# Kernel optimization log

Hardware: AMD Instinct MI355X
Metric: run time of the kernel (lower is better)

The kernel has to match this reference:

```python
import jax, jax.numpy as jnp
import numpy as np

B = 8192
NUM_NODES = 100000
EMB = 128
W1D, W2D, W3D = 64, 128, 256   # witness_dims
CODE = 128
HID = 64                        # hardcoded hidden_dim in WitnessExtractor / decoder
TOTW = W1D + W2D + W3D          # 448


def _linear_params(key, fan_in, fan_out):
    k1, k2 = jax.random.split(key)
    bound = 1.0 / np.sqrt(fan_in)
    w = jax.random.uniform(k1, (fan_out, fan_in), jnp.float32, -bound, bound)
    b = jax.random.uniform(k2, (fan_out,), jnp.float32, -bound, bound)
    return w, b


def setup_inputs() -> dict:
    key = jax.random.key(0)
    ks = jax.random.split(key, 12)
    u = jax.random.randint(ks[0], (B,), 0, NUM_NODES, dtype=jnp.int64 if jax.config.jax_enable_x64 else jnp.int32)
    v = jax.random.randint(ks[1], (B,), 0, NUM_NODES, dtype=u.dtype)
    emb = jax.random.normal(ks[2], (NUM_NODES, EMB), jnp.float32)
    e1_w1, e1_b1 = _linear_params(ks[3], 2 * EMB, HID)
    e1_w2, e1_b2 = _linear_params(ks[4], HID, W1D)
    e2_w1, e2_b1 = _linear_params(ks[5], 2 * EMB + W1D, HID)
    e2_w2, e2_b2 = _linear_params(ks[6], HID, W2D)
    e3_w1, e3_b1 = _linear_params(ks[7], 2 * EMB + W2D, HID)
    e3_w2, e3_b2 = _linear_params(ks[8], HID, W3D)
    trop_w = jax.random.normal(ks[9], (CODE, TOTW), jnp.float32)  # init_scale=1.0
    dec_w1, dec_b1 = _linear_params(ks[10], CODE, HID)
    dec_w2, dec_b2 = _linear_params(ks[11], HID, 1)
    return dict(u=u, v=v, emb=emb,
                e1_w1=e1_w1, e1_b1=e1_b1, e1_w2=e1_w2, e1_b2=e1_b2,
                e2_w1=e2_w1, e2_b1=e2_b1, e2_w2=e2_w2, e2_b2=e2_b2,
                e3_w1=e3_w1, e3_b1=e3_b1, e3_w2=e3_w2, e3_b2=e3_b2,
                trop_w=trop_w, dec_w1=dec_w1, dec_b1=dec_b1,
                dec_w2=dec_w2, dec_b2=dec_b2)


def _witness(x, w1, b1, w2, b2):
    h = jax.nn.relu(x @ w1.T + b1)
    return jax.nn.sigmoid(h @ w2.T + b2)


def reference(u, v, emb,
              e1_w1, e1_b1, e1_w2, e1_b2,
              e2_w1, e2_b1, e2_w2, e2_b2,
              e3_w1, e3_b1, e3_w2, e3_b2,
              trop_w, dec_w1, dec_b1, dec_w2, dec_b2):
    u_emb = emb[u]                               # [B, EMB]
    v_emb = emb[v]
    base = jnp.concatenate([u_emb, v_emb], axis=1)  # [B, 2*EMB]
    w1 = _witness(base, e1_w1, e1_b1, e1_w2, e1_b2)
    w2 = _witness(jnp.concatenate([base, w1], axis=1), e2_w1, e2_b1, e2_w2, e2_b2)
    w3 = _witness(jnp.concatenate([base, w2], axis=1), e3_w1, e3_b1, e3_w2, e3_b2)
    wit = jnp.concatenate([w1, w2, w3], axis=1)  # [B, TOTW]
    # tropical (min-plus) matmul: code[b,o] = min_j (wit[b,j] + trop_w[o,j])
    code = jnp.min(wit[:, None, :] + trop_w[None, :, :], axis=2)  # [B, CODE]
    h = jax.nn.relu(code @ dec_w1.T + dec_b1)
    return h @ dec_w2.T + dec_b2                 # [B, 1]
```

## Files before the change

kernel.cpp:

```cpp
#include <hip/hip_runtime.h>
#include <hip/hip_fp16.h>
#include <math.h>

#define BATCH 8192
#define EMB 128
#define TILE 16
#define NTHREADS 1024
#define NWAVES 16
#define CH 136
#define WITS 450
#define ENT_CAP 4096

#define OFF_E1W1 0
#define OFF_E1W2 16384
#define OFF_E2W1 20480
#define OFF_E2W2 40960
#define OFF_E3W1 49152
#define OFF_E3W2 73728
#define OFF_DW1  90112
#define OFF_DW2  98304
#define W_DENSE  98368

typedef __attribute__((ext_vector_type(8))) _Float16 v8h;
typedef __attribute__((ext_vector_type(4))) float v4f;

struct Smem {
    _Float16 XB[32 * CH];
    _Float16 W12C[24 * CH];
    _Float16 H[8 * CH];
    _Float16 CODE[16 * CH];
    _Float16 WITrm[TILE * WITS];
    unsigned int ent[ENT_CAP];
    unsigned int off[132];
};

__global__ __launch_bounds__(1024) void prep_kernel(
    const float* __restrict__ s0, const float* __restrict__ s1,
    const float* __restrict__ s2, const float* __restrict__ s3,
    const float* __restrict__ s4, const float* __restrict__ s5,
    const float* __restrict__ s6, const float* __restrict__ s7,
    const float* __restrict__ trop, _Float16* __restrict__ ws)
{
    const int b = blockIdx.x;
    const int tid = threadIdx.x;
    if (b < 25) {
        const int idx4 = (b * 1024 + tid) * 4;
        if (idx4 >= W_DENSE) return;
        const float* src; int off;
        if      (idx4 < OFF_E1W2) { src = s0; off = OFF_E1W1; }
        else if (idx4 < OFF_E2W1) { src = s1; off = OFF_E1W2; }
        else if (idx4 < OFF_E2W2) { src = s2; off = OFF_E2W1; }
        else if (idx4 < OFF_E3W1) { src = s3; off = OFF_E2W2; }
        else if (idx4 < OFF_E3W2) { src = s4; off = OFF_E3W1; }
        else if (idx4 < OFF_DW1)  { src = s5; off = OFF_E3W2; }
        else if (idx4 < OFF_DW2)  { src = s6; off = OFF_DW1;  }
        else                      { src = s7; off = OFF_DW2;  }
        const float4 v = *(const float4*)(src + (idx4 - off));
        _Float16* dst = ws + idx4;
        dst[0] = (_Float16)v.x; dst[1] = (_Float16)v.y;
        dst[2] = (_Float16)v.z; dst[3] = (_Float16)v.w;
    } else {
        const int lane = tid & 63;
        const int wave = tid >> 6;
        const int o = (b - 25) * 16 + wave;
        if (o >= 128) return;
        unsigned int* base = (unsigned int*)(ws + W_DENSE);
        unsigned int* counter = base + 131;

        const float* row = trop + (size_t)o * 448;
        float vals[7];
        float mn = 1e30f;
        #pragma unroll
        for (int it = 0; it < 7; ++it) {
            vals[it] = row[lane + it * 64];
            mn = fminf(mn, vals[it]);
        }
        mn = fminf(mn, __shfl_xor(mn, 1, 64));
        mn = fminf(mn, __shfl_xor(mn, 2, 64));
        mn = fminf(mn, __shfl_xor(mn, 4, 64));
        mn = fminf(mn, __shfl_xor(mn, 8, 64));
        mn = fminf(mn, __shfl_xor(mn, 16, 64));
        mn = fminf(mn, __shfl_xor(mn, 32, 64));
        const float thr = mn + 1.02f;

        unsigned long long masks[7];
        unsigned int n = 0;
        #pragma unroll
        for (int it = 0; it < 7; ++it) {
            masks[it] = __ballot(vals[it] <= thr);
            n += (unsigned)__popcll(masks[it]);
        }
        unsigned int beg = 0;
        if (lane == 0) beg = atomicAdd(counter, n);
        beg = (unsigned)__shfl((int)beg, 0, 64);
        if (lane == 0) base[o] = (n << 16) | (beg & 0xffffu);

        unsigned int done = beg;
        const unsigned long long ltmask = (1ull << lane) - 1ull;
        #pragma unroll
        for (int it = 0; it < 7; ++it) {
            const unsigned long long m = masks[it];
            if (vals[it] <= thr) {
                const unsigned int pos = done + (unsigned)__popcll(m & ltmask);
                if (pos < ENT_CAP) {
                    const unsigned short hb =
                        __builtin_bit_cast(unsigned short, (_Float16)vals[it]);
                    base[132 + pos] = ((unsigned)(lane + it * 64) << 16) | hb;
                }
            }
            done += (unsigned)__popcll(m);
        }
    }
}

template <int K, int STEPS0, int O, int ACT, bool CHUNKW, bool RMW>
__device__ __forceinline__ void dense_mfma(
    const _Float16* __restrict__ Wg, const float* __restrict__ bias,
    const _Float16* A0, const _Float16* A1,
    _Float16* OutC, _Float16* OutRM, int rmbase, int wave, int lane)
{
    constexpr int STEPS = K / 32;
    static_assert(STEPS % 2 == 0, "even steps");
    constexpr int NJOBS = O / 16;
    const int l15 = lane & 15;
    const int quad = lane >> 4;

    for (int nt = wave; nt < NJOBS; nt += NWAVES) {
        v4f c0 = {0.f, 0.f, 0.f, 0.f};
        v4f c1 = {0.f, 0.f, 0.f, 0.f};
        const _Float16* wrow = Wg + (size_t)(nt * 16 + l15) * K + quad * 8;
        #pragma unroll
        for (int s = 0; s < STEPS; s += 2) {
            const int g0 = s * 4 + quad;
            const int g1 = (s + 1) * 4 + quad;
            const _Float16* a0p = (s < STEPS0)
                ? (A0 + g0 * CH + l15 * 8)
                : (A1 + (g0 - STEPS0 * 4) * CH + l15 * 8);
            const _Float16* a1p = ((s + 1) < STEPS0)
                ? (A0 + g1 * CH + l15 * 8)
                : (A1 + (g1 - STEPS0 * 4) * CH + l15 * 8);
            const v8h a0 = *(const v8h*)a0p;
            const v8h b0 = *(const v8h*)(wrow + s * 32);
            const v8h a1 = *(const v8h*)a1p;
            const v8h b1 = *(const v8h*)(wrow + (s + 1) * 32);
            c0 = __builtin_amdgcn_mfma_f32_16x16x32_f16(a0, b0, c0, 0, 0, 0);
            c1 = __builtin_amdgcn_mfma_f32_16x16x32_f16(a1, b1, c1, 0, 0, 0);
        }
        const v4f c = c0 + c1;
        const int o = nt * 16 + l15;
        const float bs = bias[o];
        #pragma unroll
        for (int i = 0; i < 4; ++i) {
            float vv = c[i] + bs;
            if (ACT == 0) vv = fmaxf(vv, 0.f);
            else          vv = 1.f / (1.f + __expf(-vv));
            const int m = quad * 4 + i;
            const _Float16 hv = (_Float16)vv;
            if (CHUNKW) OutC[(o >> 3) * CH + m * 8 + (o & 7)] = hv;
            if (RMW)    OutRM[m * WITS + rmbase + o] = hv;
        }
    }
}

__global__ __launch_bounds__(NTHREADS, 8) void tacit_fused_kernel(
    const int* __restrict__ u, const int* __restrict__ v,
    const float* __restrict__ emb,
    const float* __restrict__ e1_b1, const float* __restrict__ e1_b2,
    const float* __restrict__ e2_b1, const float* __restrict__ e2_b2,
    const float* __restrict__ e3_b1, const float* __restrict__ e3_b2,
    const float* __restrict__ dec_b1, const float* __restrict__ dec_b2,
    const _Float16* __restrict__ ws,
    float* __restrict__ out)
{
    __shared__ Smem S;
    const int tid = threadIdx.x;
    const int lane = tid & 63;
    const int wave = tid >> 6;
    const int row0 = blockIdx.x * TILE;

    {
        const unsigned int* base = (const unsigned int*)(ws + W_DENSE);
        if (tid < 33) *(uint4*)&S.off[tid * 4] = *(const uint4*)(base + tid * 4);
        *(uint4*)&S.ent[tid * 4] = *(const uint4*)(base + 132 + tid * 4);
    }
    if (tid < 512) {
        const int row = tid & 15;
        const int kq = tid >> 4;
        const int node = (kq < 16) ? u[row0 + row] : v[row0 + row];
        const int col = (kq & 15) * 8;
        const float4 f0 = *(const float4*)(emb + (size_t)node * EMB + col);
        const float4 f1 = *(const float4*)(emb + (size_t)node * EMB + col + 4);
        v8h hv;
        hv[0] = (_Float16)f0.x; hv[1] = (_Float16)f0.y;
        hv[2] = (_Float16)f0.z; hv[3] = (_Float16)f0.w;
        hv[4] = (_Float16)f1.x; hv[5] = (_Float16)f1.y;
        hv[6] = (_Float16)f1.z; hv[7] = (_Float16)f1.w;
        *(v8h*)&S.XB[kq * CH + row * 8] = hv;
    }
    __syncthreads();

    dense_mfma<256, 8, 64, 0, true, false>(ws + OFF_E1W1, e1_b1, S.XB, nullptr,
                                           S.H, nullptr, 0, wave, lane);
    __syncthreads();
    dense_mfma<64, 2, 64, 1, true, true>(ws + OFF_E1W2, e1_b2, S.H, nullptr,
                                         S.W12C, S.WITrm, 0, wave, lane);
    __syncthreads();

    dense_mfma<320, 8, 64, 0, true, false>(ws + OFF_E2W1, e2_b1, S.XB, S.W12C,
                                           S.H, nullptr, 0, wave, lane);
    __syncthreads();
    dense_mfma<64, 2, 128, 1, true, true>(ws + OFF_E2W2, e2_b2, S.H, nullptr,
                                          S.W12C + 8 * CH, S.WITrm, 64, wave, lane);
    __syncthreads();

    dense_mfma<384, 8, 64, 0, true, false>(ws + OFF_E3W1, e3_b1, S.XB, S.W12C + 8 * CH,
                                           S.H, nullptr, 0, wave, lane);
    __syncthreads();
    dense_mfma<64, 2, 256, 1, false, true>(ws + OFF_E3W2, e3_b2, S.H, nullptr,
                                           nullptr, S.WITrm, 192, wave, lane);
    __syncthreads();

    {
        const int r = lane & 15;
        const int cp = lane >> 4;
        const _Float16* wrow = &S.WITrm[r * WITS];
        float acc[8];
        int idx[8], end8[8];
        #pragma unroll
        for (int i = 0; i < 8; ++i) {
            const int o = (wave << 3) + i;
            const unsigned int tb = S.off[o];
            const int beg = (int)(tb & 0xffffu);
            int e = beg + (int)(tb >> 16);
            e = e < ENT_CAP ? e : ENT_CAP;
            idx[i] = beg + cp;
            end8[i] = e;
            acc[i] = 1e30f;
        }
        bool any = true;
        while (any) {
            any = false;
            #pragma unroll
            for (int i = 0; i < 8; ++i) {
                if (idx[i] < end8[i]) {
                    const unsigned int cwv = S.ent[idx[i]];
                    const int j = (int)(cwv >> 16);
                    const float tv = (float)__builtin_bit_cast(
                        _Float16, (unsigned short)(cwv & 0xffffu));
                    acc[i] = fminf(acc[i], (float)wrow[j] + tv);
                    idx[i] += 4;
                    any = true;
                }
            }
        }
        #pragma unroll
        for (int i = 0; i < 8; ++i) {
            float a = acc[i];
            a = fminf(a, __shfl_xor(a, 16, 64));
            a = fminf(a, __shfl_xor(a, 32, 64));
            if (cp == 0) {
                const int o = (wave << 3) + i;
                S.CODE[(o >> 3) * CH + r * 8 + (o & 7)] = (_Float16)a;
            }
        }
    }
    __syncthreads();

    dense_mfma<128, 4, 64, 0, true, false>(ws + OFF_DW1, dec_b1, S.CODE, nullptr,
                                           S.H, nullptr, 0, wave, lane);
    __syncthreads();

    if (tid < 64) {
        const int r = lane & 15;
        const int part = lane >> 4;
        const _Float16* w2 = ws + OFF_DW2;
        float s = 0.f;
        #pragma unroll
        for (int q = 0; q < 2; ++q) {
            const int c = part + q * 4;
            const v8h hr = *(const v8h*)(&S.H[c * CH + r * 8]);
            const v8h wr = *(const v8h*)(w2 + c * 8);
            #pragma unroll
            for (int t = 0; t < 8; ++t) s += (float)hr[t] * (float)wr[t];
        }
        s += __shfl_xor(s, 16, 64);
        s += __shfl_xor(s, 32, 64);
        if (part == 0) out[row0 + r] = s + dec_b2[0];
    }
}

extern "C" void kernel_launch(void* const* d_in, const int* in_sizes, int n_in,
                              void* d_out, int out_size, void* d_ws, size_t ws_size,
                              hipStream_t stream) {
    const int*   u      = (const int*)d_in[0];
    const int*   v      = (const int*)d_in[1];
    const float* emb    = (const float*)d_in[2];
    const float* e1_w1  = (const float*)d_in[3];
    const float* e1_b1  = (const float*)d_in[4];
    const float* e1_w2  = (const float*)d_in[5];
    const float* e1_b2  = (const float*)d_in[6];
    const float* e2_w1  = (const float*)d_in[7];
    const float* e2_b1  = (const float*)d_in[8];
    const float* e2_w2  = (const float*)d_in[9];
    const float* e2_b2  = (const float*)d_in[10];
    const float* e3_w1  = (const float*)d_in[11];
    const float* e3_b1  = (const float*)d_in[12];
    const float* e3_w2  = (const float*)d_in[13];
    const float* e3_b2  = (const float*)d_in[14];
    const float* trop_w = (const float*)d_in[15];
    const float* dec_w1 = (const float*)d_in[16];
    const float* dec_b1 = (const float*)d_in[17];
    const float* dec_w2 = (const float*)d_in[18];
    const float* dec_b2 = (const float*)d_in[19];
    float* out = (float*)d_out;
    _Float16* ws = (_Float16*)d_ws;

    hipMemsetAsync((char*)d_ws + (size_t)W_DENSE * 2 + 131 * 4, 0, 4, stream);

    prep_kernel<<<33, 1024, 0, stream>>>(
        e1_w1, e1_w2, e2_w1, e2_w2, e3_w1, e3_w2, dec_w1, dec_w2, trop_w, ws);

    tacit_fused_kernel<<<BATCH / TILE, NTHREADS, 0, stream>>>(
        u, v, emb,
        e1_b1, e1_b2, e2_b1, e2_b2, e3_b1, e3_b2, dec_b1, dec_b2,
        ws, out);
}
```

Measured before the change: 145.5 us.

## Halve batch tile to 8 rows and read tropical table from global

Shrinks each block to 8 batch rows and 512 threads and drops the per-block LDS copy of the sparse tropical table. The tropical min-plus loop now reads offsets and entries straight from the workspace in global memory, with the lane split and shuffle reductions adjusted. The aim is a smaller shared-memory footprint and more resident blocks per CU, and no per-block table-staging cost. In exchange, the 16-row MFMA tiles are likely half empty, which doubles dense work per real row, and table lookups now go through the cache hierarchy instead of LDS.

Result: slower. 157.8 us (+8.5%).

```diff
diff --git a/kernel.cpp b/kernel.cpp
--- a/kernel.cpp
+++ b/kernel.cpp
@@ -4,9 +4,9 @@
 
 #define BATCH 8192
 #define EMB 128
-#define TILE 16
-#define NTHREADS 1024
-#define NWAVES 16
+#define TILE 8
+#define NTHREADS 512
+#define NWAVES 8
 #define CH 136
 #define WITS 450
 #define ENT_CAP 4096
@@ -29,10 +29,9 @@
     _Float16 W12C[24 * CH];
     _Float16 H[8 * CH];
     _Float16 CODE[16 * CH];
-    _Float16 WITrm[TILE * WITS];
-    unsigned int ent[ENT_CAP];
-    unsigned int off[132];
+    _Float16 WITrm[16 * WITS];
 };
+static_assert(sizeof(Smem) <= 37 * 1024, "4 blocks/CU requires <=40KB");
 
 __global__ __launch_bounds__(1024) void prep_kernel(
     const float* __restrict__ s0, const float* __restrict__ s1,
@@ -177,25 +176,18 @@
     const int lane = tid & 63;
     const int wave = tid >> 6;
     const int row0 = blockIdx.x * TILE;
+    const unsigned int* cbase = (const unsigned int*)(ws + W_DENSE);
 
     {
-        const unsigned int* base = (const unsigned int*)(ws + W_DENSE);
-        if (tid < 33) *(uint4*)&S.off[tid * 4] = *(const uint4*)(base + tid * 4);
-        *(uint4*)&S.ent[tid * 4] = *(const uint4*)(base + 132 + tid * 4);
-    }
-    if (tid < 512) {
-        const int row = tid & 15;
-        const int kq = tid >> 4;
-        const int node = (kq < 16) ? u[row0 + row] : v[row0 + row];
-        const int col = (kq & 15) * 8;
-        const float4 f0 = *(const float4*)(emb + (size_t)node * EMB + col);
-        const float4 f1 = *(const float4*)(emb + (size_t)node * EMB + col + 4);
-        v8h hv;
-        hv[0] = (_Float16)f0.x; hv[1] = (_Float16)f0.y;
-        hv[2] = (_Float16)f0.z; hv[3] = (_Float16)f0.w;
-        hv[4] = (_Float16)f1.x; hv[5] = (_Float16)f1.y;
-        hv[6] = (_Float16)f1.z; hv[7] = (_Float16)f1.w;
-        *(v8h*)&S.XB[kq * CH + row * 8] = hv;
+        const int lrow = tid >> 5;
+        const int c2 = tid & 31;
+        const int r = lrow >> 1;
+        const int uvhalf = lrow & 1;
+        const int node = uvhalf ? v[row0 + r] : u[row0 + r];
+        const float4 f = *(const float4*)(emb + (size_t)node * EMB + c2 * 4);
+        _Float16* dst = &S.XB[(uvhalf * 16 + (c2 >> 1)) * CH + r * 8 + (c2 & 1) * 4];
+        dst[0] = (_Float16)f.x; dst[1] = (_Float16)f.y;
+        dst[2] = (_Float16)f.z; dst[3] = (_Float16)f.w;
     }
     __syncthreads();
 
@@ -221,46 +213,50 @@
     __syncthreads();
 
     {
-        const int r = lane & 15;
-        const int cp = lane >> 4;
+        const int r = lane & 7;
+        const int cp = lane >> 3;
         const _Float16* wrow = &S.WITrm[r * WITS];
-        float acc[8];
-        int idx[8], end8[8];
-        #pragma unroll
-        for (int i = 0; i < 8; ++i) {
-            const int o = (wave << 3) + i;
-            const unsigned int tb = S.off[o];
-            const int beg = (int)(tb & 0xffffu);
-            int e = beg + (int)(tb >> 16);
-            e = e < ENT_CAP ? e : ENT_CAP;
-            idx[i] = beg + cp;
-            end8[i] = e;
-            acc[i] = 1e30f;
-        }
-        bool any = true;
-        while (any) {
-            any = false;
+        #pragma unroll
+        for (int h = 0; h < 2; ++h) {
+            float acc[8];
+            int idx[8], end8[8];
             #pragma unroll
             for (int i = 0; i < 8; ++i) {
-                if (idx[i] < end8[i]) {
-                    const unsigned int cwv = S.ent[idx[i]];
-                    const int j = (int)(cwv >> 16);
-                    const float tv = (float)__builtin_bit_cast(
-                        _Float16, (unsigned short)(cwv & 0xffffu));
-                    acc[i] = fminf(acc[i], (float)wrow[j] + tv);
-                    idx[i] += 4;
-                    any = true;
+                const int o = (wave << 4) + (h << 3) + i;
+                const unsigned int tb = cbase[o];
+                const int beg = (int)(tb & 0xffffu);
+                int e = beg + (int)(tb >> 16);
+                e = e < ENT_CAP ? e : ENT_CAP;
+                idx[i] = beg + cp;
+                end8[i] = e;
+                acc[i] = 1e30f;
+            }
+            bool any = true;
+            while (any) {
+                any = false;
+                #pragma unroll
+                for (int i = 0; i < 8; ++i) {
+                    if (idx[i] < end8[i]) {
+                        const unsigned int cwv = cbase[132 + idx[i]];
+                        const int j = (int)(cwv >> 16);
+                        const float tv = (float)__builtin_bit_cast(
+                            _Float16, (unsigned short)(cwv & 0xffffu));
+                        acc[i] = fminf(acc[i], (float)wrow[j] + tv);
+                        idx[i] += 8;
+                        any = true;
+                    }
                 }
             }
-        }
-        #pragma unroll
-        for (int i = 0; i < 8; ++i) {
-            float a = acc[i];
-            a = fminf(a, __shfl_xor(a, 16, 64));
-            a = fminf(a, __shfl_xor(a, 32, 64));
-            if (cp == 0) {
-                const int o = (wave << 3) + i;
-                S.CODE[(o >> 3) * CH + r * 8 + (o & 7)] = (_Float16)a;
+            #pragma unroll
+            for (int i = 0; i < 8; ++i) {
+                float a = acc[i];
+                a = fminf(a, __shfl_xor(a, 8, 64));
+                a = fminf(a, __shfl_xor(a, 16, 64));
+                a = fminf(a, __shfl_xor(a, 32, 64));
+                if (cp == 0) {
+                    const int o = (wave << 4) + (h << 3) + i;
+                    S.CODE[(o >> 3) * CH + r * 8 + (o & 7)] = (_Float16)a;
+                }
             }
         }
     }
@@ -271,18 +267,15 @@
     __syncthreads();
 
     if (tid < 64) {
-        const int r = lane & 15;
-        const int part = lane >> 4;
+        const int r = lane & 7;
+        const int part = lane >> 3;
         const _Float16* w2 = ws + OFF_DW2;
+        const v8h hr = *(const v8h*)(&S.H[part * CH + r * 8]);
+        const v8h wr = *(const v8h*)(w2 + part * 8);
         float s = 0.f;
         #pragma unroll
-        for (int q = 0; q < 2; ++q) {
-            const int c = part + q * 4;
-            const v8h hr = *(const v8h*)(&S.H[c * CH + r * 8]);
-            const v8h wr = *(const v8h*)(w2 + c * 8);
-            #pragma unroll
-            for (int t = 0; t < 8; ++t) s += (float)hr[t] * (float)wr[t];
-        }
+        for (int t = 0; t < 8; ++t) s += (float)hr[t] * (float)wr[t];
+        s += __shfl_xor(s, 8, 64);
         s += __shfl_xor(s, 16, 64);
         s += __shfl_xor(s, 32, 64);
         if (part == 0) out[row0 + r] = s + dec_b2[0];
```
